# Kernel optimization log

Hardware: AMD Instinct MI355X
Metric: run time of the kernel (lower is better)

The kernel has to match this reference:

```python
import jax, jax.numpy as jnp
import numpy as np

D = 192
HEADS = 4
HD = D // HEADS
R = 3  # correlation radius actually used in forward_level
NDISP = (2 * R + 1) ** 2  # 49
T = 3  # frames -> 2 consecutive pairs
ITERS = 4


def layer_norm(x, w, b, eps=1e-5):
    m = jnp.mean(x, axis=-1, keepdims=True)
    v = jnp.var(x, axis=-1, keepdims=True)
    return (x - m) / jnp.sqrt(v + eps) * w + b


def mha(x, in_w, in_b, out_w, out_b):
    # torch nn.MultiheadAttention, batch_first, self-attention
    B, N, _ = x.shape
    qkv = x @ in_w.T + in_b
    q, k, v = jnp.split(qkv, 3, axis=-1)
    q = q.reshape(B, N, HEADS, HD).transpose(0, 2, 1, 3) * (1.0 / float(np.sqrt(HD)))
    k = k.reshape(B, N, HEADS, HD).transpose(0, 2, 1, 3)
    v = v.reshape(B, N, HEADS, HD).transpose(0, 2, 1, 3)
    att = jax.nn.softmax(jnp.einsum('bhqd,bhkd->bhqk', q, k), axis=-1)
    y = jnp.einsum('bhqk,bhkd->bhqd', att, v).transpose(0, 2, 1, 3).reshape(B, N, D)
    return y @ out_w.T + out_b


def tblock(x, p):
    ln1w, ln1b, inw, inb, ow, ob, ln2w, ln2b, w1, b1, w2, b2 = p
    x = x + mha(layer_norm(x, ln1w, ln1b), inw, inb, ow, ob)
    h = layer_norm(x, ln2w, ln2b)
    h = jax.nn.gelu(h @ w1.T + b1, approximate=False) @ w2.T + b2
    return x + h


def local_corr(f1, f2):
    C = f1.shape[1]
    scale = 1.0 / float(np.sqrt(C))
    outs = []
    for dy in range(-R, R + 1):
        for dx in range(-R, R + 1):
            f2s = jnp.roll(f2, (dy, dx), axis=(2, 3))
            outs.append(jnp.sum(f1 * f2s, axis=1) * scale)
    return jnp.stack(outs, axis=1)


def grid_sample_bilinear_border(img, grid):
    # img: B,C,H,W; grid: B,Ho,Wo,2 with (x,y) in [-1,1]; align_corners=True, border padding
    B, C, H, W = img.shape
    x = jnp.clip((grid[..., 0] + 1.0) * 0.5 * (W - 1), 0.0, W - 1)
    y = jnp.clip((grid[..., 1] + 1.0) * 0.5 * (H - 1), 0.0, H - 1)
    x0 = jnp.floor(x); y0 = jnp.floor(y)
    x1 = jnp.minimum(x0 + 1, W - 1); y1 = jnp.minimum(y0 + 1, H - 1)
    wx = (x - x0)[:, None]; wy = (y - y0)[:, None]
    imgf = img.reshape(B, C, H * W)
    Ho, Wo = x.shape[1], x.shape[2]
    def gather(yy, xx):
        idx = (yy * W + xx).astype(jnp.int32).reshape(B, 1, Ho * Wo)
        return jnp.take_along_axis(imgf, idx, axis=2).reshape(B, C, Ho, Wo)
    v00 = gather(y0, x0); v01 = gather(y0, x1)
    v10 = gather(y1, x0); v11 = gather(y1, x1)
    return v00 * (1 - wx) * (1 - wy) + v01 * wx * (1 - wy) + v10 * (1 - wx) * wy + v11 * wx * wy


def warp(img, flow):
    # flow in pixels, Bx2xHxW
    B, C, H, W = img.shape
    xs = jnp.linspace(-1.0, 1.0, W); ys = jnp.linspace(-1.0, 1.0, H)
    gx, gy = jnp.meshgrid(xs, ys)  # each (H, W), 'xy' indexing
    base = jnp.stack([gx, gy], axis=-1)[None]
    off = jnp.stack([flow[:, 0] * (2.0 / max(W - 1, 1)),
                     flow[:, 1] * (2.0 / max(H - 1, 1))], axis=-1)
    return grid_sample_bilinear_border(img, base + off)


def upsample2x_align(img):
    # F.interpolate(scale_factor=2, mode='bilinear', align_corners=True)
    B, C, H, W = img.shape
    Ho, Wo = 2 * H, 2 * W
    xs = jnp.linspace(-1.0, 1.0, Wo); ys = jnp.linspace(-1.0, 1.0, Ho)
    gx, gy = jnp.meshgrid(xs, ys)
    grid = jnp.broadcast_to(jnp.stack([gx, gy], axis=-1)[None], (B, Ho, Wo, 2))
    return grid_sample_bilinear_border(img, grid)


def conv2d(x, w, b):
    y = jax.lax.conv_general_dilated(x, w, (1, 1), ((1, 1), (1, 1)),
                                     dimension_numbers=('NCHW', 'OIHW', 'NCHW'))
    return y + b[None, :, None, None]


def _forward(feats_l1, feats_l2, feats_l3, tok_w, tok_b,
             lcm_ln1_w, lcm_ln1_b, lcm_in_w, lcm_in_b, lcm_out_w, lcm_out_b,
             lcm_ln2_w, lcm_ln2_b, lcm_mlp_w1, lcm_mlp_b1, lcm_mlp_w2, lcm_mlp_b2,
             gtr_ln1_w, gtr_ln1_b, gtr_in_w, gtr_in_b, gtr_out_w, gtr_out_b,
             gtr_ln2_w, gtr_ln2_b, gtr_mlp_w1, gtr_mlp_b1, gtr_mlp_w2, gtr_mlp_b2,
             head_w1, head_b1, head_w2, head_b2,
             ref1_w1, ref1_b1, ref1_w2, ref1_b2,
             ref0_w1, ref0_b1, ref0_w2, ref0_b2):
    feats = [[feats_l1[t] for t in range(T)],
             [feats_l2[t] for t in range(T)],
             [feats_l3[t] for t in range(T)]]
    # ---- CostTokenizer ----
    tokens = []
    for lvl in range(3):
        toks = []
        for k in range(T - 1):
            corr = local_corr(feats[lvl][k], feats[lvl][k + 1])
            toks.append(jnp.einsum('bchw,dc->bdhw', corr, tok_w[lvl]) + tok_b[lvl][None, :, None, None])
        tokens.append(toks)
    lcm_p = [(lcm_ln1_w[i], lcm_ln1_b[i], lcm_in_w[i], lcm_in_b[i], lcm_out_w[i], lcm_out_b[i],
              lcm_ln2_w[i], lcm_ln2_b[i], lcm_mlp_w1[i], lcm_mlp_b1[i], lcm_mlp_w2[i], lcm_mlp_b2[i])
             for i in range(lcm_ln1_w.shape[0])]
    gtr_p = [(gtr_ln1_w[i], gtr_ln1_b[i], gtr_in_w[i], gtr_in_b[i], gtr_out_w[i], gtr_out_b[i],
              gtr_ln2_w[i], gtr_ln2_b[i], gtr_mlp_w1[i], gtr_mlp_b1[i], gtr_mlp_w2[i], gtr_mlp_b2[i])
             for i in range(gtr_ln1_w.shape[0])]
    # ---- LatentCostMemory (EMA state; .detach() -> stop_gradient; state resets when N changes) ----
    state = None
    latent = []
    for toks in tokens:
        lvl_lat = []
        for tok in toks:
            B_, Dd, H, W = tok.shape
            x = tok.reshape(B_, Dd, H * W).transpose(0, 2, 1)  # b (h w) d
            for p in lcm_p:
                x = tblock(x, p)
            if state is None or state.shape[1] != x.shape[1]:
                state = jax.lax.stop_gradient(x)
            x = 0.8 * x + 0.2 * state
            state = jax.lax.stop_gradient(x)
            lvl_lat.append(x.transpose(0, 2, 1))  # b d n
        latent.append(lvl_lat)
    H8, W8 = feats[1][0].shape[-2:]
    coarse = []
    for lat in latent[1]:
        x = lat.transpose(0, 2, 1)
        for p in gtr_p:
            x = tblock(x, p)
        fv = jax.nn.gelu(x @ head_w1.T + head_b1, approximate=False) @ head_w2.T + head_b2
        coarse.append(fv.transpose(0, 2, 1).reshape(-1, 2, H8, W8))
    # ---- MSRecurrentDecoder ----
    outs = []
    for k, f8 in enumerate(coarse):
        cur = f8
        for _ in range(ITERS):
            w10 = warp(feats[1][k + 1], cur)
            x = jnp.concatenate([feats[1][k], cur, w10], axis=1)
            cur = cur + conv2d(jax.nn.gelu(conv2d(x, ref1_w1, ref1_b1), approximate=False), ref1_w2, ref1_b2)
        cur2 = upsample2x_align(cur)
        for _ in range(ITERS):
            w10 = warp(feats[0][k + 1], cur2)
            x = jnp.concatenate([feats[0][k], cur2, w10], axis=1)
            cur2 = cur2 + conv2d(jax.nn.gelu(conv2d(x, ref0_w1, ref0_b1), approximate=False), ref0_w2, ref0_b2)
        outs.append(cur2)
    return jnp.stack(outs)  # [pairs, B, 2, H/4, W/4]


def setup_inputs():
    key = jax.random.key(0)
    ks = iter(jax.random.split(key, 64))
    def rn(shape, s=1.0):
        return jax.random.normal(next(ks), shape, dtype=jnp.float32) * s
    B = 1
    inp = {}
    inp['feats_l1'] = rn((T, B, 64, 64, 64))
    inp['feats_l2'] = rn((T, B, 128, 32, 32))
    inp['feats_l3'] = rn((T, B, 192, 16, 16))
    inp['tok_w'] = rn((3, D, NDISP), 0.02)
    inp['tok_b'] = rn((3, D), 0.02)
    for pre, n in (('lcm', 6), ('gtr', 2)):
        inp[pre + '_ln1_w'] = jnp.ones((n, D), jnp.float32)
        inp[pre + '_ln1_b'] = jnp.zeros((n, D), jnp.float32)
        inp[pre + '_in_w'] = rn((n, 3 * D, D), 0.02)
        inp[pre + '_in_b'] = rn((n, 3 * D), 0.02)
        inp[pre + '_out_w'] = rn((n, D, D), 0.02)
        inp[pre + '_out_b'] = rn((n, D), 0.02)
        inp[pre + '_ln2_w'] = jnp.ones((n, D), jnp.float32)
        inp[pre + '_ln2_b'] = jnp.zeros((n, D), jnp.float32)
        inp[pre + '_mlp_w1'] = rn((n, 4 * D, D), 0.02)
        inp[pre + '_mlp_b1'] = rn((n, 4 * D), 0.02)
        inp[pre + '_mlp_w2'] = rn((n, D, 4 * D), 0.02)
        inp[pre + '_mlp_b2'] = rn((n, D), 0.02)
    inp['head_w1'] = rn((D, D), 0.02); inp['head_b1'] = rn((D,), 0.02)
    inp['head_w2'] = rn((2, D), 0.02); inp['head_b2'] = rn((2,), 0.02)
    inp['ref1_w1'] = rn((128, 258, 3, 3), 0.02); inp['ref1_b1'] = rn((128,), 0.02)
    inp['ref1_w2'] = rn((2, 128, 3, 3), 0.02); inp['ref1_b2'] = rn((2,), 0.02)
    inp['ref0_w1'] = rn((64, 130, 3, 3), 0.02); inp['ref0_b1'] = rn((64,), 0.02)
    inp['ref0_w2'] = rn((2, 64, 3, 3), 0.02); inp['ref0_b2'] = rn((2,), 0.02)
    return inp


def reference(feats_l1, feats_l2, feats_l3, tok_w, tok_b,
              lcm_ln1_w, lcm_ln1_b, lcm_in_w, lcm_in_b, lcm_out_w, lcm_out_b,
              lcm_ln2_w, lcm_ln2_b, lcm_mlp_w1, lcm_mlp_b1, lcm_mlp_w2, lcm_mlp_b2,
              gtr_ln1_w, gtr_ln1_b, gtr_in_w, gtr_in_b, gtr_out_w, gtr_out_b,
              gtr_ln2_w, gtr_ln2_b, gtr_mlp_w1, gtr_mlp_b1, gtr_mlp_w2, gtr_mlp_b2,
              head_w1, head_b1, head_w2, head_b2,
              ref1_w1, ref1_b1, ref1_w2, ref1_b2,
              ref0_w1, ref0_b1, ref0_w2, ref0_b2):
    return _forward(feats_l1, feats_l2, feats_l3, tok_w, tok_b,
                    lcm_ln1_w, lcm_ln1_b, lcm_in_w, lcm_in_b, lcm_out_w, lcm_out_b,
                    lcm_ln2_w, lcm_ln2_b, lcm_mlp_w1, lcm_mlp_b1, lcm_mlp_w2, lcm_mlp_b2,
                    gtr_ln1_w, gtr_ln1_b, gtr_in_w, gtr_in_b, gtr_out_w, gtr_out_b,
                    gtr_ln2_w, gtr_ln2_b, gtr_mlp_w1, gtr_mlp_b1, gtr_mlp_w2, gtr_mlp_b2,
                    head_w1, head_b1, head_w2, head_b2,
                    ref1_w1, ref1_b1, ref1_w2, ref1_b2,
                    ref0_w1, ref0_b1, ref0_w2, ref0_b2)
```

## Files before the change

kernel.cpp:

```cpp
#include <hip/hip_runtime.h>
#include <hip/hip_bf16.h>

typedef __hip_bfloat16 bf16;
typedef short bf16x8 __attribute__((ext_vector_type(8)));
typedef float f32x4 __attribute__((ext_vector_type(4)));

#define DEV __device__ __forceinline__

DEV float bf2f(bf16 v) { return __bfloat162float(v); }
DEV bf16 f2bf(float v) { return __float2bfloat16(v); }
DEV unsigned short bfr(float f) {
  bf16 h = __float2bfloat16(f);
  return *reinterpret_cast<unsigned short*>(&h);
}
DEV float shf(unsigned short u) {
  unsigned int x = ((unsigned int)u) << 16;
  return *reinterpret_cast<float*>(&x);
}
DEV float gelu_exact(float x) { return 0.5f * x * (1.0f + erff(x * 0.70710678118654752f)); }

DEV float ldw(const void* p, long i, int isb) {
  return isb ? __bfloat162float(((const bf16*)p)[i]) : ((const float*)p)[i];
}

__global__ void k_detect(const unsigned short* __restrict__ u, int* __restrict__ flag) {
  __shared__ int bad;
  if (threadIdx.x == 0) bad = 0;
  __syncthreads();
  for (int i = threadIdx.x; i < 8192; i += 256) {
    int expo = (u[i] >> 7) & 0xFF;
    if (expo >= 138) atomicOr(&bad, 1);
  }
  __syncthreads();
  if (threadIdx.x == 0) *flag = bad ? 0 : 1;
}
__global__ void k_setone(int* p) { *p = 1; }

__global__ void k_cvt(const void* __restrict__ s, float* __restrict__ d, int n,
                      const int* __restrict__ fl) {
  int isb = *fl;
  int i = blockIdx.x * blockDim.x + threadIdx.x;
  if (i < n) d[i] = ldw(s, i, isb);
}

__global__ void k_zerosh(unsigned short* __restrict__ p, int n8) {
  int i = blockIdx.x * blockDim.x + threadIdx.x;
  if (i < n8) { uint4 z = {0, 0, 0, 0}; *(uint4*)(p + (long)i * 8) = z; }
}

__global__ void k_padtokw(const void* __restrict__ tw, bf16* __restrict__ dst,
                          const int* __restrict__ fl) {
  int isb = *fl;
  int i = blockIdx.x * blockDim.x + threadIdx.x;
  if (i >= 12288) return;
  int n = i >> 6, k = i & 63;
  float v = (k < 49) ? ldw(tw, 9408 + (long)n * 49 + k, isb) : 0.0f;
  dst[i] = f2bf(v);
}

__global__ void k_packw(const void* __restrict__ src, bf16* __restrict__ dst,
                        int OC, int C, int ICT, int NP, int ICP, int n,
                        const int* __restrict__ fl) {
  int isb = *fl;
  int i = blockIdx.x * blockDim.x + threadIdx.x;
  if (i >= n) return;
  int s = i / (NP * ICP);
  int r = i - s * NP * ICP;
  int oc = r / ICP, icp = r - oc * ICP;
  float v = 0.0f;
  if (oc < OC) {
    int ic = -1;
    if (icp < C) ic = icp;
    else if (icp < 2 * C) ic = icp - C + C + 2;
    else if (icp < 2 * C + 2) ic = icp - 2 * C + C;
    if (ic >= 0 && ic < ICT) v = ldw(src, ((long)oc * ICT + ic) * 9 + s, isb);
  }
  dst[i] = f2bf(v);
}

__global__ void k_trans_feats(const void* __restrict__ in, bf16* __restrict__ Fp,
                              int F, int C, int HW, const int* __restrict__ fl) {
  int isb = *fl;
  int cpg = C >> 3;
  int n = F * HW * cpg;
  int i = blockIdx.x * blockDim.x + threadIdx.x;
  if (i >= n) return;
  int p = i % HW;
  int rem = i / HW;
  int c8 = rem % cpg;
  int f = rem / cpg;
  long base = (long)f * C * HW + (long)(c8 * 8) * HW + p;
  union { unsigned short u[8]; uint4 v; } pk;
#pragma unroll
  for (int j = 0; j < 8; ++j) pk.u[j] = bfr(ldw(in, base + (long)j * HW, isb));
  *(uint4*)((unsigned short*)Fp + ((long)f * HW + p) * C + c8 * 8) = pk.v;
}

template <int MW, int NT>
__global__ __launch_bounds__(256) void k_conv_warp(
    const bf16* __restrict__ Fp, const float* __restrict__ flow, int C, int ICP,
    const bf16* __restrict__ Wp, const float* __restrict__ bias,
    void* __restrict__ out, int NOUT, int H, int W, int lgW) {
  constexpr int NWN = 4 / MW;
  constexpr int BM = MW * 16;
  constexpr int BN = NWN * NT * 16;
  __shared__ unsigned short Asm[102][40];
  __shared__ unsigned short Wsm[9 * BN][40];
  int tid = threadIdx.x;
  int wv = tid >> 6, ln = tid & 63, quad = ln >> 4, l16 = ln & 15;
  int wm = wv % MW, wn = wv / MW;
  int n0 = blockIdx.x * BN;
  int m0 = blockIdx.y * BM;
  int b = blockIdx.z;
  int HW = H * W;
  int CW = (BM < W) ? BM : W;
  int lgCW = (CW == 64) ? 6 : 5;
  int RO = (BM > W) ? (BM >> lgW) : 1;
  int ACW = CW + 2;
  int AR = (RO + 2) * ACW;
  int py0 = m0 >> lgW;
  int px0 = m0 & (W - 1);
  const unsigned short* fcur = (const unsigned short*)Fp + (long)b * HW * C;
  const unsigned short* fnxt = (const unsigned short*)Fp + (long)(b + 1) * HW * C;
  const float* fl = flow + (long)b * 2 * HW;
  int nk = ICP >> 5;
  f32x4 acc[NT] = {};
  int mm_local = wm * 16 + l16;
  int plr = mm_local >> lgCW;
  int plc = mm_local & (CW - 1);
  for (int kc = 0; kc < nk; ++kc) {
    int chbase = kc * 32;
    for (int i = tid; i < AR * 4; i += 256) {
      int r = i >> 2, c4 = i & 3;
      int sr = r / ACW, sc = r - sr * ACW;
      int py = py0 + sr - 1, px = px0 + sc - 1;
      uint4 val = {0, 0, 0, 0};
      if (py >= 0 && py < H && px >= 0 && px < W) {
        int p = py * W + px;
        int ch = chbase + c4 * 8;
        if (ch < C) {
          val = *(const uint4*)(fcur + (long)p * C + ch);
        } else if (ch < 2 * C) {
          float fx = fl[p], fy = fl[HW + p];
          float x = fminf(fmaxf((float)px + fx, 0.0f), (float)(W - 1));
          float y = fminf(fmaxf((float)py + fy, 0.0f), (float)(H - 1));
          int x0 = (int)floorf(x), y0 = (int)floorf(y);
          int x1 = min(x0 + 1, W - 1), y1 = min(y0 + 1, H - 1);
          float wx = x - (float)x0, wy = y - (float)y0;
          float w00 = (1 - wx) * (1 - wy), w01 = wx * (1 - wy);
          float w10 = (1 - wx) * wy, w11 = wx * wy;
          int c = ch - C;
          union { unsigned short u[8]; uint4 v; } a = { .v = *(const uint4*)(fnxt + (long)(y0 * W + x0) * C + c) };
          union { unsigned short u[8]; uint4 v; } bb = { .v = *(const uint4*)(fnxt + (long)(y0 * W + x1) * C + c) };
          union { unsigned short u[8]; uint4 v; } cc = { .v = *(const uint4*)(fnxt + (long)(y1 * W + x0) * C + c) };
          union { unsigned short u[8]; uint4 v; } dd = { .v = *(const uint4*)(fnxt + (long)(y1 * W + x1) * C + c) };
          union { unsigned short u[8]; uint4 v; } o;
#pragma unroll
          for (int j = 0; j < 8; ++j) {
            float v = shf(a.u[j]) * w00 + shf(bb.u[j]) * w01 + shf(cc.u[j]) * w10 + shf(dd.u[j]) * w11;
            o.u[j] = bfr(v);
          }
          val = o.v;
        } else if (ch == 2 * C) {
          union { unsigned short u[8]; uint4 v; } o = { .v = {0, 0, 0, 0} };
          o.u[0] = bfr(fl[p]);
          o.u[1] = bfr(fl[HW + p]);
          val = o.v;
        }
      }
      *(uint4*)&Asm[r][c4 * 8] = val;
    }
    for (int i = tid; i < 9 * BN * 4; i += 256) {
      int r = i >> 2, c4 = i & 3;
      int s = r / BN, nl = r - s * BN;
      long g = ((long)s * NOUT + n0 + nl) * ICP + kc * 32 + c4 * 8;
      *(uint4*)&Wsm[r][c4 * 8] = *(const uint4*)((const unsigned short*)Wp + g);
    }
    __syncthreads();
#pragma unroll
    for (int s = 0; s < 9; ++s) {
      int ky = s / 3, kx = s - ky * 3;
      bf16x8 af = *(const bf16x8*)&Asm[(plr + ky) * ACW + plc + kx][quad * 8];
#pragma unroll
      for (int nt = 0; nt < NT; ++nt) {
        bf16x8 wf = *(const bf16x8*)&Wsm[s * BN + (wn * NT + nt) * 16 + l16][quad * 8];
        acc[nt] = __builtin_amdgcn_mfma_f32_16x16x32_bf16(af, wf, acc[nt], 0, 0, 0);
      }
    }
    __syncthreads();
  }
  int Wp2 = W + 2;
#pragma unroll
  for (int nt = 0; nt < NT; ++nt) {
    int n = n0 + (wn * NT + nt) * 16 + l16;
    float bv = bias[n];
#pragma unroll
    for (int r = 0; r < 4; ++r) {
      int mmo = m0 + wm * 16 + quad * 4 + r;
      int py = mmo >> lgW, px = mmo & (W - 1);
      float v = gelu_exact(acc[nt][r] + bv);
      ((unsigned short*)out)[((long)b * (H + 2) * Wp2 + (long)(py + 1) * Wp2 + px + 1) * NOUT + n]
          = bfr(v);
    }
  }
}

template <int MW, int NT, int MODE>
__global__ __launch_bounds__(256) void k_conv_mfma(
    const bf16* __restrict__ Ap, int ICP, const bf16* __restrict__ Wp,
    const float* __restrict__ bias, const float* __restrict__ res,
    void* __restrict__ out, int NOUT, int H, int W, int lgW) {
  constexpr int NWN = 4 / MW;
  constexpr int BM = MW * 16;
  constexpr int BN = NWN * NT * 16;
  __shared__ unsigned short Asm[198][40];
  __shared__ unsigned short Wsm[9 * BN][40];
  int tid = threadIdx.x;
  int wv = tid >> 6, ln = tid & 63, quad = ln >> 4, l16 = ln & 15;
  int wm = wv % MW, wn = wv / MW;
  int n0 = blockIdx.x * BN;
  int m0 = blockIdx.y * BM;
  int b = blockIdx.z;
  int Wp2 = W + 2;
  int CW = (BM < W) ? BM : W;
  int lgCW = (CW == 64) ? 6 : 5;
  int RO = (BM > W) ? (BM >> lgW) : 1;
  int ACW = CW + 2;
  int AR = (RO + 2) * ACW;
  int py0 = m0 >> lgW;
  int px0 = m0 & (W - 1);
  const unsigned short* A = (const unsigned short*)Ap + (long)b * (H + 2) * Wp2 * ICP;
  int NPr = (MODE == 0) ? NOUT : 16;
  int nk = ICP >> 5;
  f32x4 acc[NT] = {};
  int mm_local = wm * 16 + l16;
  int plr = mm_local >> lgCW;
  int plc = mm_local & (CW - 1);
  for (int kc = 0; kc < nk; ++kc) {
    for (int i = tid; i < AR * 4; i += 256) {
      int r = i >> 2, c4 = i & 3;
      int sr = r / ACW, sc = r - sr * ACW;
      long g = ((long)(py0 + sr) * Wp2 + px0 + sc) * ICP + kc * 32 + c4 * 8;
      *(uint4*)&Asm[r][c4 * 8] = *(const uint4*)(A + g);
    }
    for (int i = tid; i < 9 * BN * 4; i += 256) {
      int r = i >> 2, c4 = i & 3;
      int s = r / BN, nl = r - s * BN;
      long g = ((long)s * NPr + n0 + nl) * ICP + kc * 32 + c4 * 8;
      *(uint4*)&Wsm[r][c4 * 8] = *(const uint4*)((const unsigned short*)Wp + g);
    }
    __syncthreads();
#pragma unroll
    for (int s = 0; s < 9; ++s) {
      int ky = s / 3, kx = s - ky * 3;
      bf16x8 af = *(const bf16x8*)&Asm[(plr + ky) * ACW + plc + kx][quad * 8];
#pragma unroll
      for (int nt = 0; nt < NT; ++nt) {
        bf16x8 wf = *(const bf16x8*)&Wsm[s * BN + (wn * NT + nt) * 16 + l16][quad * 8];
        acc[nt] = __builtin_amdgcn_mfma_f32_16x16x32_bf16(af, wf, acc[nt], 0, 0, 0);
      }
    }
    __syncthreads();
  }
  if (MODE == 0) {
#pragma unroll
    for (int nt = 0; nt < NT; ++nt) {
      int n = n0 + (wn * NT + nt) * 16 + l16;
      float bv = bias[n];
#pragma unroll
      for (int r = 0; r < 4; ++r) {
        int mmo = m0 + wm * 16 + quad * 4 + r;
        int py = mmo >> lgW, px = mmo & (W - 1);
        float v = gelu_exact(acc[nt][r] + bv);
        ((unsigned short*)out)[((long)b * (H + 2) * Wp2 + (long)(py + 1) * Wp2 + px + 1) * NOUT + n]
            = bfr(v);
      }
    }
  } else {
    int n = l16;
    if (wn == 0 && n < 2) {
      float bv = bias[n];
      int HW = H * W;
#pragma unroll
      for (int r = 0; r < 4; ++r) {
        int mmo = m0 + wm * 16 + quad * 4 + r;
        float v = acc[0][r] + bv + res[(long)b * 2 * HW + (long)n * HW + mmo];
        ((float*)out)[(long)b * 2 * HW + (long)n * HW + mmo] = v;
      }
    }
  }
}

__global__ void k_corr(const bf16* __restrict__ Fp2, bf16* __restrict__ corrT) {
  __shared__ unsigned short f1r[128];
  int p = blockIdx.x;
  int b = blockIdx.y;
  int t = threadIdx.x;
  const unsigned short* f1 = (const unsigned short*)Fp2 + ((long)b * 1024 + p) * 128;
  if (t < 16) *(uint4*)&f1r[t * 8] = *(const uint4*)(f1 + t * 8);
  __syncthreads();
  long rowo = ((long)b * 1024 + p) * 64;
  if (t < 49) {
    int dy = t / 7 - 3, dx = t % 7 - 3;
    int h = p >> 5, w = p & 31;
    int p2 = (((h - dy) & 31) << 5) | ((w - dx) & 31);
    const unsigned short* f2 = (const unsigned short*)Fp2 + ((long)(b + 1) * 1024 + p2) * 128;
    float s = 0.0f;
    for (int c = 0; c < 128; c += 8) {
      union { unsigned short u[8]; uint4 v; } av = { .v = *(const uint4*)&f1r[c] };
      union { unsigned short u[8]; uint4 v; } bv = { .v = *(const uint4*)(f2 + c) };
#pragma unroll
      for (int j = 0; j < 8; ++j) s += shf(av.u[j]) * shf(bv.u[j]);
    }
    corrT[rowo + t] = f2bf(s * 0.08838834764831845f);
  } else {
    corrT[rowo + t] = f2bf(0.0f);
  }
}

template <int KT, int BM, int ACT, bool HASRES, int AMODE, int OUTBF, int VT>
__global__ __launch_bounds__(256) void k_gemm_mfma2(
    const void* __restrict__ A, const void* __restrict__ W, long woff,
    const void* __restrict__ bias, long boff, const int* __restrict__ flb,
    const float* __restrict__ res, void* __restrict__ C,
    int M, int N, const int* __restrict__ fl,
    const unsigned short* __restrict__ mop, const float* __restrict__ mml,
    bf16* __restrict__ vtout,
    const void* __restrict__ lnw, long lnwoff,
    const void* __restrict__ lnb, long lnboff) {
  (void)M;
  int isb = *fl;
  constexpr int NKC = ((KT < 192) ? KT : 192) >> 5;
  constexpr int WM = (BM == 64) ? 4 : 2;
  constexpr int NTW = (BM == 64) ? 4 : 2;
  constexpr int LPR = 256 / BM;
  constexpr int EPL = 192 / LPR;
  __shared__ unsigned short Asm[NKC][BM][40];
  __shared__ unsigned short Wsm[NKC][64][40];
  int tid = threadIdx.x;
  int wv = tid >> 6, ln = tid & 63;
  int quad = ln >> 4, l16 = ln & 15;
  int wm = wv % WM, wn = wv / WM;
  int m0 = blockIdx.y * BM, n0 = blockIdx.x * 64;
  f32x4 acc[NTW] = {};
  for (int s0 = 0; s0 < KT; s0 += 192) {
    if (s0) __syncthreads();
    for (int i = tid; i < NKC * 256; i += 256) {
      int c4 = i & 3, r = (i >> 2) & 63, kc = i >> 8;
      long eo = woff + (long)(n0 + r) * KT + s0 + kc * 32 + c4 * 8;
      if (isb) {
        *(uint4*)&Wsm[kc][r][c4 * 8] = *(const uint4*)((const unsigned short*)W + eo);
      } else {
        const float* wp = (const float*)W + eo;
        float4 w0 = *(const float4*)wp;
        float4 w1 = *(const float4*)(wp + 4);
        union { unsigned short u[8]; uint4 v; } pk;
        pk.u[0] = bfr(w0.x); pk.u[1] = bfr(w0.y); pk.u[2] = bfr(w0.z); pk.u[3] = bfr(w0.w);
        pk.u[4] = bfr(w1.x); pk.u[5] = bfr(w1.y); pk.u[6] = bfr(w1.z); pk.u[7] = bfr(w1.w);
        *(uint4*)&Wsm[kc][r][c4 * 8] = pk.v;
      }
    }
    if constexpr (AMODE == 1) {
      for (int i = tid; i < NKC * BM * 4; i += 256) {
        int c4 = i & 3, r = (i >> 2) % BM, kc = i / (BM * 4);
        const unsigned short* ap =
            (const unsigned short*)A + (long)(m0 + r) * KT + s0 + kc * 32 + c4 * 8;
        *(uint4*)&Asm[kc][r][c4 * 8] = *(const uint4*)ap;
      }
    } else if constexpr (AMODE == 0) {
      for (int i = tid; i < NKC * BM * 4; i += 256) {
        int c4 = i & 3, r = (i >> 2) % BM, kc = i / (BM * 4);
        const float* ap = (const float*)A + (long)(m0 + r) * KT + s0 + kc * 32 + c4 * 8;
        float4 a0 = *(const float4*)ap;
        float4 a1 = *(const float4*)(ap + 4);
        union { unsigned short u[8]; uint4 v; } pk;
        pk.u[0] = bfr(a0.x); pk.u[1] = bfr(a0.y); pk.u[2] = bfr(a0.z); pk.u[3] = bfr(a0.w);
        pk.u[4] = bfr(a1.x); pk.u[5] = bfr(a1.y); pk.u[6] = bfr(a1.z); pk.u[7] = bfr(a1.w);
        *(uint4*)&Asm[kc][r][c4 * 8] = pk.v;
      }
    } else if constexpr (AMODE == 3) {
      int row = tid / LPR, j = tid % LPR;
      const float* xr = (const float*)A + (long)(m0 + row) * 192 + j * EPL;
      float av[EPL];
#pragma unroll
      for (int q4 = 0; q4 < EPL / 4; ++q4) {
        float4 v = *(const float4*)(xr + q4 * 4);
        av[q4 * 4 + 0] = v.x; av[q4 * 4 + 1] = v.y;
        av[q4 * 4 + 2] = v.z; av[q4 * 4 + 3] = v.w;
      }
      float sum = 0.0f;
#pragma unroll
      for (int q = 0; q < EPL; ++q) sum += av[q];
#pragma unroll
      for (int o = 1; o < LPR; o <<= 1) sum += __shfl_xor(sum, o);
      float mean = sum * (1.0f / 192.0f);
      float vs = 0.0f;
#pragma unroll
      for (int q = 0; q < EPL; ++q) { float d = av[q] - mean; vs += d * d; }
#pragma unroll
      for (int o = 1; o < LPR; o <<= 1) vs += __shfl_xor(vs, o);
      float rstd = rsqrtf(vs * (1.0f / 192.0f) + 1e-5f);
#pragma unroll
      for (int g = 0; g < EPL / 8; ++g) {
        int k = j * EPL + g * 8;
        union { unsigned short u[8]; uint4 v; } pk;
#pragma unroll
        for (int e = 0; e < 8; ++e) {
          float gg = ldw(lnw, lnwoff + k + e, isb);
          float bb = ldw(lnb, lnboff + k + e, isb);
          pk.u[e] = bfr((av[g * 8 + e] - mean) * rstd * gg + bb);
        }
        *(uint4*)&Asm[k >> 5][row][k & 31] = pk.v;
      }
    } else {
      int row = tid / LPR, j = tid % LPR;
      int m = m0 + row;
      int rr = m & 1023, bb = m >> 10;
#pragma unroll
      for (int g = 0; g < EPL / 8; ++g) {
        int k = j * EPL + g * 8;
        int h = k / 48;
        int d0 = k - h * 48;
        long idx[4];
        float ms[4], ls[4];
        float Ms = -1e30f;
#pragma unroll
        for (int s = 0; s < 4; ++s) {
          idx[s] = (((long)s * 2 + bb) * 4 + h) * 1024 + rr;
          ms[s] = mml[idx[s] * 2];
          ls[s] = mml[idx[s] * 2 + 1];
          Ms = fmaxf(Ms, ms[s]);
        }
        float e[4], L = 0.0f;
#pragma unroll
        for (int s = 0; s < 4; ++s) { e[s] = __expf(ms[s] - Ms); L += ls[s] * e[s]; }
        float invL = 1.0f / L;
        union { unsigned short u[8]; uint4 v; } pk;
#pragma unroll
        for (int e2 = 0; e2 < 8; ++e2) {
          float o = 0.0f;
#pragma unroll
          for (int s = 0; s < 4; ++s) o += shf(mop[idx[s] * 48 + d0 + e2]) * e[s];
// ... 188 lines not shown
    if (isb) ((bf16*)out)[i] = f2bf(cur2[i]);
    else ((float*)out)[i] = cur2[i];
  }
}

extern "C" void kernel_launch(void* const* d_in, const int* in_sizes, int n_in,
                              void* d_out, int out_size, void* d_ws, size_t ws_size,
                              hipStream_t stream) {
  const void* feats_l1 = d_in[0];
  const void* feats_l2 = d_in[1];
  const void* tok_w = d_in[3];
  const void* tok_b = d_in[4];
  const void* lcm_ln1_w = d_in[5];
  const void* lcm_ln1_b = d_in[6];
  const void* lcm_in_w  = d_in[7];
  const void* lcm_in_b  = d_in[8];
  const void* lcm_out_w = d_in[9];
  const void* lcm_out_b = d_in[10];
  const void* lcm_ln2_w = d_in[11];
  const void* lcm_ln2_b = d_in[12];
  const void* lcm_mlp_w1 = d_in[13];
  const void* lcm_mlp_b1 = d_in[14];
  const void* lcm_mlp_w2 = d_in[15];
  const void* lcm_mlp_b2 = d_in[16];
  const void* gtr_ln1_w = d_in[17];
  const void* gtr_ln1_b = d_in[18];
  const void* gtr_in_w  = d_in[19];
  const void* gtr_in_b  = d_in[20];
  const void* gtr_out_w = d_in[21];
  const void* gtr_out_b = d_in[22];
  const void* gtr_ln2_w = d_in[23];
  const void* gtr_ln2_b = d_in[24];
  const void* gtr_mlp_w1 = d_in[25];
  const void* gtr_mlp_b1 = d_in[26];
  const void* gtr_mlp_w2 = d_in[27];
  const void* gtr_mlp_b2 = d_in[28];
  const void* head_w1 = d_in[29];
  const void* head_b1 = d_in[30];
  const void* head_w2 = d_in[31];
  const void* head_b2 = d_in[32];
  const void* ref1_w1 = d_in[33];
  const void* ref1_b1 = d_in[34];
  const void* ref1_w2 = d_in[35];
  const void* ref1_b2 = d_in[36];
  const void* ref0_w1 = d_in[37];
  const void* ref0_b1 = d_in[38];
  const void* ref0_w2 = d_in[39];
  const void* ref0_b2 = d_in[40];
  (void)ws_size; (void)n_in; (void)in_sizes; (void)out_size;

  int* flag = (int*)d_ws;
  int* oneflag = (int*)d_ws + 2;
  float* wsf = (float*)d_ws;
  float* F2   = wsf + 16;
  float* rA   = F2 + 393216;
  float* rX   = rA + 786432;
  float* rT   = rX + 393216;
  float* rY   = rT + 393216;
  float* big  = rY + 393216;
  float* fv   = big + 1572864;
  float* cur  = fv + 4096;
  float* cur2 = cur + 4096;
  float* cb1a = cur2 + 16384;
  float* cb1b = cb1a + 128;
  float* cb0a = cb1b + 16;
  float* cb0b = cb0a + 64;
  bf16* wtok  = (bf16*)(cb0b + 16);
  float* wpk  = cb0b + 16 + 6144;
  bf16* w1p1 = (bf16*)wpk;
  bf16* w1p2 = (bf16*)(wpk + 165888);
  bf16* w0p1 = (bf16*)(wpk + 175104);
  bf16* w0p2 = (bf16*)(wpk + 221184);

  float* x = rX;
  bf16* corrTb = (bf16*)big;
  bf16* qkvbb  = (bf16*)big;
  bf16* vtb    = (bf16*)(big + 655360);
  bf16* hidb   = (bf16*)big;
  unsigned short* opart = (unsigned short*)rA;
  float* mlbuf = rY;
  float* headh = rT;
  bf16* mid0p = (bf16*)rT;
  bf16* mid1p = (bf16*)rY;
  bf16* Fp2   = (bf16*)(big + 851968);
  bf16* Fp1   = (bf16*)(big + 1048576);

  k_detect<<<1, 256, 0, stream>>>((const unsigned short*)feats_l1, flag);
  k_setone<<<1, 1, 0, stream>>>(oneflag);
  k_cvt<<<1, 256, 0, stream>>>(ref1_b1, cb1a, 128, flag);
  k_cvt<<<1, 256, 0, stream>>>(ref1_b2, cb1b, 2, flag);
  k_cvt<<<1, 256, 0, stream>>>(ref0_b1, cb0a, 64, flag);
  k_cvt<<<1, 256, 0, stream>>>(ref0_b2, cb0b, 2, flag);
  k_padtokw<<<48, 256, 0, stream>>>(tok_w, wtok, flag);
  k_packw<<<1296, 256, 0, stream>>>(ref1_w1, w1p1, 128, 128, 258, 128, 288, 331776, flag);
  k_packw<<<72, 256, 0, stream>>>(ref1_w2, w1p2, 2, 128, 128, 16, 128, 18432, flag);
  k_packw<<<360, 256, 0, stream>>>(ref0_w1, w0p1, 64, 64, 130, 64, 160, 92160, flag);
  k_packw<<<36, 256, 0, stream>>>(ref0_w2, w0p2, 2, 64, 64, 16, 64, 9216, flag);
  k_trans_feats<<<192, 256, 0, stream>>>(feats_l2, Fp2, 3, 128, 1024, flag);
  k_trans_feats<<<384, 256, 0, stream>>>(feats_l1, Fp1, 3, 64, 4096, flag);

  k_corr<<<dim3(1024, 2), 64, 0, stream>>>(Fp2, corrTb);
  k_gemm_mfma2<64, 32, 0, false, 1, 0, 0><<<dim3(3, 64), 256, 0, stream>>>(
      corrTb, wtok, 0, tok_b, 192, flag, nullptr, x, 2048, 192, oneflag,
      nullptr, nullptr, nullptr, nullptr, 0, nullptr, 0);

  auto run_block = [&](const void* ln1w, long o1, const void* ln1b, long o2,
                       const void* inw, long o3, const void* inb, long o4,
                       const void* ow, long o5, const void* ob, long o6,
                       const void* ln2w, long o7, const void* ln2b, long o8,
                       const void* w1, long o9, const void* b1, long o10,
                       const void* w2, long o11, const void* b2, long o12) {
    k_gemm_mfma2<192, 64, 0, false, 3, 1, 1><<<dim3(9, 32), 256, 0, stream>>>(
        x, inw, o3, inb, o4, flag, nullptr, qkvbb, 2048, 576, flag,
        nullptr, nullptr, vtb, ln1w, o1, ln1b, o2);
    k_attn_mfma<<<dim3(64, 4, 2), 256, 0, stream>>>(qkvbb, vtb, opart, mlbuf);
    k_gemm_mfma2<192, 32, 0, true, 2, 0, 0><<<dim3(3, 64), 256, 0, stream>>>(
        nullptr, ow, o5, ob, o6, flag, x, x, 2048, 192, flag,
        opart, mlbuf, nullptr, nullptr, 0, nullptr, 0);
    k_gemm_mfma2<192, 64, 1, false, 3, 1, 0><<<dim3(12, 32), 256, 0, stream>>>(
        x, w1, o9, b1, o10, flag, nullptr, hidb, 2048, 768, flag,
        nullptr, nullptr, nullptr, ln2w, o7, ln2b, o8);
    k_gemm_mfma2<768, 32, 0, true, 1, 0, 0><<<dim3(3, 64), 256, 0, stream>>>(
        hidb, w2, o11, b2, o12, flag, x, x, 2048, 192, flag,
        nullptr, nullptr, nullptr, nullptr, 0, nullptr, 0);
  };

  for (int i = 0; i < 6; ++i) {
    run_block(lcm_ln1_w, (long)i * 192, lcm_ln1_b, (long)i * 192,
              lcm_in_w, (long)i * 110592, lcm_in_b, (long)i * 576,
              lcm_out_w, (long)i * 36864, lcm_out_b, (long)i * 192,
              lcm_ln2_w, (long)i * 192, lcm_ln2_b, (long)i * 192,
              lcm_mlp_w1, (long)i * 147456, lcm_mlp_b1, (long)i * 768,
              lcm_mlp_w2, (long)i * 147456, lcm_mlp_b2, (long)i * 192);
  }
  k_ema<<<768, 256, 0, stream>>>(x);

  for (int i = 0; i < 2; ++i) {
    run_block(gtr_ln1_w, (long)i * 192, gtr_ln1_b, (long)i * 192,
              gtr_in_w, (long)i * 110592, gtr_in_b, (long)i * 576,
              gtr_out_w, (long)i * 36864, gtr_out_b, (long)i * 192,
              gtr_ln2_w, (long)i * 192, gtr_ln2_b, (long)i * 192,
              gtr_mlp_w1, (long)i * 147456, gtr_mlp_b1, (long)i * 768,
              gtr_mlp_w2, (long)i * 147456, gtr_mlp_b2, (long)i * 192);
  }

  k_gemm_mfma2<192, 32, 1, false, 0, 0, 0><<<dim3(3, 64), 256, 0, stream>>>(
      x, head_w1, 0, head_b1, 0, flag, nullptr, headh, 2048, 192, flag,
      nullptr, nullptr, nullptr, nullptr, 0, nullptr, 0);
  k_head2<<<1024, 256, 0, stream>>>(headh, head_w2, head_b2, cur, flag);

  k_zerosh<<<768, 256, 0, stream>>>((unsigned short*)rT, 196608);

  for (int it = 0; it < 4; ++it) {
    k_conv_warp<2, 2><<<dim3(2, 32, 2), 256, 0, stream>>>(
        Fp2, cur, 128, 288, w1p1, cb1a, mid1p, 128, 32, 32, 5);
    k_conv_mfma<4, 1, 1><<<dim3(1, 16, 2), 256, 0, stream>>>(
        mid1p, 128, w1p2, cb1b, cur, cur, 2, 32, 32, 5);
  }
  k_upsample<<<64, 256, 0, stream>>>(cur, cur2);

  for (int it = 0; it < 4; ++it) {
    k_conv_warp<2, 2><<<dim3(1, 128, 2), 256, 0, stream>>>(
        Fp1, cur2, 64, 160, w0p1, cb0a, mid0p, 64, 64, 64, 6);
    k_conv_mfma<4, 1, 1><<<dim3(1, 64, 2), 256, 0, stream>>>(
        mid0p, 64, w0p2, cb0b, cur2, cur2, 2, 64, 64, 6);
  }

  k_out<<<64, 256, 0, stream>>>(cur2, d_out, flag);
}
```

Measured before the change: 1.029 ms.

## Pipeline warp-conv tile loads through registers and replace final conv with wave dot

```diff
diff --git a/kernel.cpp b/kernel.cpp
--- a/kernel.cpp
+++ b/kernel.cpp
@@ -96,198 +96,217 @@
   *(uint4*)((unsigned short*)Fp + ((long)f * HW + p) * C + c8 * 8) = pk.v;
 }
 
-template <int MW, int NT>
-__global__ __launch_bounds__(256) void k_conv_warp(
-    const bf16* __restrict__ Fp, const float* __restrict__ flow, int C, int ICP,
+template <int C, int ICP, int NOUT, int WW, int LGW>
+__global__ __launch_bounds__(256) void k_conv_warp2(
+    const bf16* __restrict__ Fp, const float* __restrict__ flow,
     const bf16* __restrict__ Wp, const float* __restrict__ bias,
-    void* __restrict__ out, int NOUT, int H, int W, int lgW) {
-  constexpr int NWN = 4 / MW;
-  constexpr int BM = MW * 16;
-  constexpr int BN = NWN * NT * 16;
-  __shared__ unsigned short Asm[102][40];
-  __shared__ unsigned short Wsm[9 * BN][40];
+    bf16* __restrict__ out) {
+  constexpr int HH = WW;
+  constexpr int HW = HH * WW;
+  constexpr int ACW = 34;
+  constexpr int AR = 3 * ACW;
+  constexpr int NK = ICP / 32;
+  constexpr int NWI = 5;
+  __shared__ unsigned short Asm[AR][40];
+  __shared__ unsigned short Wsm[9 * 32][40];
   int tid = threadIdx.x;
   int wv = tid >> 6, ln = tid & 63, quad = ln >> 4, l16 = ln & 15;
-  int wm = wv % MW, wn = wv / MW;
-  int n0 = blockIdx.x * BN;
-  int m0 = blockIdx.y * BM;
-  int b = blockIdx.z;
-  int HW = H * W;
-  int CW = (BM < W) ? BM : W;
-  int lgCW = (CW == 64) ? 6 : 5;
-  int RO = (BM > W) ? (BM >> lgW) : 1;
-  int ACW = CW + 2;
-  int AR = (RO + 2) * ACW;
-  int py0 = m0 >> lgW;
-  int px0 = m0 & (W - 1);
+  int wm = wv & 1, wn = wv >> 1;
+  int n0 = blockIdx.x * 32, m0 = blockIdx.y * 32, b = blockIdx.z;
+  int py0 = m0 >> LGW, px0 = m0 & (WW - 1);
   const unsigned short* fcur = (const unsigned short*)Fp + (long)b * HW * C;
   const unsigned short* fnxt = (const unsigned short*)Fp + (long)(b + 1) * HW * C;
   const float* fl = flow + (long)b * 2 * HW;
-  int nk = ICP >> 5;
-  f32x4 acc[NT] = {};
-  int mm_local = wm * 16 + l16;
-  int plr = mm_local >> lgCW;
-  int plc = mm_local & (CW - 1);
-  for (int kc = 0; kc < nk; ++kc) {
-    int chbase = kc * 32;
-    for (int i = tid; i < AR * 4; i += 256) {
-      int r = i >> 2, c4 = i & 3;
-      int sr = r / ACW, sc = r - sr * ACW;
-      int py = py0 + sr - 1, px = px0 + sc - 1;
-      uint4 val = {0, 0, 0, 0};
-      if (py >= 0 && py < H && px >= 0 && px < W) {
-        int p = py * W + px;
-        int ch = chbase + c4 * 8;
-        if (ch < C) {
-          val = *(const uint4*)(fcur + (long)p * C + ch);
-        } else if (ch < 2 * C) {
-          float fx = fl[p], fy = fl[HW + p];
-          float x = fminf(fmaxf((float)px + fx, 0.0f), (float)(W - 1));
-          float y = fminf(fmaxf((float)py + fy, 0.0f), (float)(H - 1));
-          int x0 = (int)floorf(x), y0 = (int)floorf(y);
-          int x1 = min(x0 + 1, W - 1), y1 = min(y0 + 1, H - 1);
-          float wx = x - (float)x0, wy = y - (float)y0;
-          float w00 = (1 - wx) * (1 - wy), w01 = wx * (1 - wy);
-          float w10 = (1 - wx) * wy, w11 = wx * wy;
-          int c = ch - C;
-          union { unsigned short u[8]; uint4 v; } a = { .v = *(const uint4*)(fnxt + (long)(y0 * W + x0) * C + c) };
-          union { unsigned short u[8]; uint4 v; } bb = { .v = *(const uint4*)(fnxt + (long)(y0 * W + x1) * C + c) };
-          union { unsigned short u[8]; uint4 v; } cc = { .v = *(const uint4*)(fnxt + (long)(y1 * W + x0) * C + c) };
-          union { unsigned short u[8]; uint4 v; } dd = { .v = *(const uint4*)(fnxt + (long)(y1 * W + x1) * C + c) };
-          union { unsigned short u[8]; uint4 v; } o;
-#pragma unroll
-          for (int j = 0; j < 8; ++j) {
-            float v = shf(a.u[j]) * w00 + shf(bb.u[j]) * w01 + shf(cc.u[j]) * w10 + shf(dd.u[j]) * w11;
-            o.u[j] = bfr(v);
-          }
-          val = o.v;
-        } else if (ch == 2 * C) {
-          union { unsigned short u[8]; uint4 v; } o = { .v = {0, 0, 0, 0} };
-          o.u[0] = bfr(fl[p]);
-          o.u[1] = bfr(fl[HW + p]);
-          val = o.v;
+  int c4 = tid & 3;
+  const uint4 Z4 = {0, 0, 0, 0};
+  int rr_[2], ipp[2];
+  bool ivalid[2], iin[2];
+  float w00[2], w01[2], w10[2], w11[2], ifx[2], ify[2];
+  const unsigned short *g00[2], *g01[2], *g10[2], *g11[2];
+#pragma unroll
+  for (int j = 0; j < 2; ++j) {
+    int idx = tid + j * 256;
+    ivalid[j] = idx < AR * 4;
+    int r = idx >> 2;
+    rr_[j] = r;
+    int sr = r / ACW, sc = r - sr * ACW;
+    int py = py0 + sr - 1, px = px0 + sc - 1;
+    bool in = ivalid[j] && py >= 0 && py < HH && px >= 0 && px < WW;
+    iin[j] = in;
+    int p = in ? (py * WW + px) : 0;
+    ipp[j] = p;
+    float fx = 0.0f, fy = 0.0f;
+    if (in) { fx = fl[p]; fy = fl[HW + p]; }
+    ifx[j] = fx; ify[j] = fy;
+    float x = fminf(fmaxf((float)px + fx, 0.0f), (float)(WW - 1));
+    float y = fminf(fmaxf((float)py + fy, 0.0f), (float)(HH - 1));
+    int x0 = (int)floorf(x), y0 = (int)floorf(y);
+    int x1 = min(x0 + 1, WW - 1), y1 = min(y0 + 1, HH - 1);
+    float wx = x - (float)x0, wy = y - (float)y0;
+    w00[j] = (1 - wx) * (1 - wy); w01[j] = wx * (1 - wy);
+    w10[j] = (1 - wx) * wy;       w11[j] = wx * wy;
+    g00[j] = fnxt + (long)(y0 * WW + x0) * C;
+    g01[j] = fnxt + (long)(y0 * WW + x1) * C;
+    g10[j] = fnxt + (long)(y1 * WW + x0) * C;
+    g11[j] = fnxt + (long)(y1 * WW + x1) * C;
+  }
+  uint4 fa[2] = {};
+  uint4 qa[2], qb[2], qc[2], qd[2];
+  uint4 wreg[NWI];
+  auto ldW = [&](int kc) {
+#pragma unroll
+    for (int j = 0; j < NWI; ++j) {
+      int idx = tid + j * 256;
+      if (idx < 9 * 32 * 4) {
+        int r = idx >> 2, cw = idx & 3;
+        int s = r >> 5, nl = r & 31;
+        wreg[j] = *(const uint4*)((const unsigned short*)Wp +
+                                  ((long)s * NOUT + n0 + nl) * ICP + kc * 32 + cw * 8);
+      }
+    }
+  };
+  auto stW = [&]() {
+#pragma unroll
+    for (int j = 0; j < NWI; ++j) {
+      int idx = tid + j * 256;
+      if (idx < 9 * 32 * 4) {
+        int r = idx >> 2, cw = idx & 3;
+        *(uint4*)&Wsm[r][cw * 8] = wreg[j];
+      }
+    }
+  };
+  auto ldA = [&](int kc) {
+    int chb = kc * 32;
+    if (chb < C) {
+#pragma unroll
+      for (int j = 0; j < 2; ++j) {
+        if (iin[j]) fa[j] = *(const uint4*)(fcur + (long)ipp[j] * C + chb + c4 * 8);
+        else fa[j] = Z4;
+      }
+    } else if (chb < 2 * C) {
+      int c = chb - C + c4 * 8;
+#pragma unroll
+      for (int j = 0; j < 2; ++j) {
+        if (iin[j]) {
+          qa[j] = *(const uint4*)(g00[j] + c);
+          qb[j] = *(const uint4*)(g01[j] + c);
+          qc[j] = *(const uint4*)(g10[j] + c);
+          qd[j] = *(const uint4*)(g11[j] + c);
         }
       }
-      *(uint4*)&Asm[r][c4 * 8] = val;
-    }
-    for (int i = tid; i < 9 * BN * 4; i += 256) {
-      int r = i >> 2, c4 = i & 3;
-      int s = r / BN, nl = r - s * BN;
-      long g = ((long)s * NOUT + n0 + nl) * ICP + kc * 32 + c4 * 8;
-      *(uint4*)&Wsm[r][c4 * 8] = *(const uint4*)((const unsigned short*)Wp + g);
-    }
+    }
+  };
+  auto stA = [&](int kc) {
+    int chb = kc * 32;
+    if (chb < C) {
+#pragma unroll
+      for (int j = 0; j < 2; ++j)
+        if (ivalid[j]) *(uint4*)&Asm[rr_[j]][c4 * 8] = fa[j];
+    } else if (chb < 2 * C) {
+#pragma unroll
+      for (int j = 0; j < 2; ++j) {
+        if (!ivalid[j]) continue;
+        uint4 val = Z4;
+        if (iin[j]) {
+          union { unsigned short u[8]; uint4 v; } A_ = { .v = qa[j] };
+          union { unsigned short u[8]; uint4 v; } B_ = { .v = qb[j] };
+          union { unsigned short u[8]; uint4 v; } C_ = { .v = qc[j] };
+          union { unsigned short u[8]; uint4 v; } D_ = { .v = qd[j] };
+          union { unsigned short u[8]; uint4 v; } O_;
+#pragma unroll
+          for (int e = 0; e < 8; ++e)
+            O_.u[e] = bfr(shf(A_.u[e]) * w00[j] + shf(B_.u[e]) * w01[j] +
+                          shf(C_.u[e]) * w10[j] + shf(D_.u[e]) * w11[j]);
+          val = O_.v;
+        }
+        *(uint4*)&Asm[rr_[j]][c4 * 8] = val;
+      }
+    } else {
+#pragma unroll
+      for (int j = 0; j < 2; ++j) {
+        if (!ivalid[j]) continue;
+        union { unsigned short u[8]; uint4 v; } O_ = { .v = {0, 0, 0, 0} };
+        if (iin[j] && c4 == 0) { O_.u[0] = bfr(ifx[j]); O_.u[1] = bfr(ify[j]); }
+        *(uint4*)&Asm[rr_[j]][c4 * 8] = O_.v;
+      }
+    }
+  };
+  f32x4 acc = {};
+  int mml = wm * 16 + l16;
+  ldW(0);
+  ldA(0);
+#pragma unroll
+  for (int kc = 0; kc < NK; ++kc) {
+    stW();
+    stA(kc);
     __syncthreads();
+    if (kc + 1 < NK) { ldW(kc + 1); ldA(kc + 1); }
 #pragma unroll
     for (int s = 0; s < 9; ++s) {
       int ky = s / 3, kx = s - ky * 3;
-      bf16x8 af = *(const bf16x8*)&Asm[(plr + ky) * ACW + plc + kx][quad * 8];
-#pragma unroll
-      for (int nt = 0; nt < NT; ++nt) {
-        bf16x8 wf = *(const bf16x8*)&Wsm[s * BN + (wn * NT + nt) * 16 + l16][quad * 8];
-        acc[nt] = __builtin_amdgcn_mfma_f32_16x16x32_bf16(af, wf, acc[nt], 0, 0, 0);
-      }
+      bf16x8 af = *(const bf16x8*)&Asm[ky * ACW + mml + kx][quad * 8];
+      bf16x8 wf = *(const bf16x8*)&Wsm[s * 32 + wn * 16 + l16][quad * 8];
+      acc = __builtin_amdgcn_mfma_f32_16x16x32_bf16(af, wf, acc, 0, 0, 0);
     }
     __syncthreads();
   }
-  int Wp2 = W + 2;
-#pragma unroll
-  for (int nt = 0; nt < NT; ++nt) {
-    int n = n0 + (wn * NT + nt) * 16 + l16;
-    float bv = bias[n];
-#pragma unroll
-    for (int r = 0; r < 4; ++r) {
-      int mmo = m0 + wm * 16 + quad * 4 + r;
-      int py = mmo >> lgW, px = mmo & (W - 1);
-      float v = gelu_exact(acc[nt][r] + bv);
-      ((unsigned short*)out)[((long)b * (H + 2) * Wp2 + (long)(py + 1) * Wp2 + px + 1) * NOUT + n]
-          = bfr(v);
-    }
-  }
-}
-
-template <int MW, int NT, int MODE>
-__global__ __launch_bounds__(256) void k_conv_mfma(
-    const bf16* __restrict__ Ap, int ICP, const bf16* __restrict__ Wp,
-    const float* __restrict__ bias, const float* __restrict__ res,
-    void* __restrict__ out, int NOUT, int H, int W, int lgW) {
-  constexpr int NWN = 4 / MW;
-  constexpr int BM = MW * 16;
-  constexpr int BN = NWN * NT * 16;
-  __shared__ unsigned short Asm[198][40];
-  __shared__ unsigned short Wsm[9 * BN][40];
-  int tid = threadIdx.x;
-  int wv = tid >> 6, ln = tid & 63, quad = ln >> 4, l16 = ln & 15;
-  int wm = wv % MW, wn = wv / MW;
-  int n0 = blockIdx.x * BN;
-  int m0 = blockIdx.y * BM;
-  int b = blockIdx.z;
-  int Wp2 = W + 2;
-  int CW = (BM < W) ? BM : W;
-  int lgCW = (CW == 64) ? 6 : 5;
-  int RO = (BM > W) ? (BM >> lgW) : 1;
-  int ACW = CW + 2;
-  int AR = (RO + 2) * ACW;
-  int py0 = m0 >> lgW;
-  int px0 = m0 & (W - 1);
-  const unsigned short* A = (const unsigned short*)Ap + (long)b * (H + 2) * Wp2 * ICP;
-  int NPr = (MODE == 0) ? NOUT : 16;
-  int nk = ICP >> 5;
-  f32x4 acc[NT] = {};
-  int mm_local = wm * 16 + l16;
-  int plr = mm_local >> lgCW;
-  int plc = mm_local & (CW - 1);
-  for (int kc = 0; kc < nk; ++kc) {
-    for (int i = tid; i < AR * 4; i += 256) {
-      int r = i >> 2, c4 = i & 3;
-      int sr = r / ACW, sc = r - sr * ACW;
-      long g = ((long)(py0 + sr) * Wp2 + px0 + sc) * ICP + kc * 32 + c4 * 8;
-      *(uint4*)&Asm[r][c4 * 8] = *(const uint4*)(A + g);
-    }
-    for (int i = tid; i < 9 * BN * 4; i += 256) {
-      int r = i >> 2, c4 = i & 3;
-      int s = r / BN, nl = r - s * BN;
-      long g = ((long)s * NPr + n0 + nl) * ICP + kc * 32 + c4 * 8;
-      *(uint4*)&Wsm[r][c4 * 8] = *(const uint4*)((const unsigned short*)Wp + g);
-    }
-    __syncthreads();
-#pragma unroll
-    for (int s = 0; s < 9; ++s) {
-      int ky = s / 3, kx = s - ky * 3;
-      bf16x8 af = *(const bf16x8*)&Asm[(plr + ky) * ACW + plc + kx][quad * 8];
-#pragma unroll
-      for (int nt = 0; nt < NT; ++nt) {
-        bf16x8 wf = *(const bf16x8*)&Wsm[s * BN + (wn * NT + nt) * 16 + l16][quad * 8];
-        acc[nt] = __builtin_amdgcn_mfma_f32_16x16x32_bf16(af, wf, acc[nt], 0, 0, 0);
-      }
-    }
-    __syncthreads();
-  }
-  if (MODE == 0) {
-#pragma unroll
-    for (int nt = 0; nt < NT; ++nt) {
-      int n = n0 + (wn * NT + nt) * 16 + l16;
-      float bv = bias[n];
-#pragma unroll
-      for (int r = 0; r < 4; ++r) {
-        int mmo = m0 + wm * 16 + quad * 4 + r;
-        int py = mmo >> lgW, px = mmo & (W - 1);
-        float v = gelu_exact(acc[nt][r] + bv);
-        ((unsigned short*)out)[((long)b * (H + 2) * Wp2 + (long)(py + 1) * Wp2 + px + 1) * NOUT + n]
-            = bfr(v);
-      }
-    }
-  } else {
-    int n = l16;
-    if (wn == 0 && n < 2) {
-      float bv = bias[n];
-      int HW = H * W;
-#pragma unroll
-      for (int r = 0; r < 4; ++r) {
-        int mmo = m0 + wm * 16 + quad * 4 + r;
-        float v = acc[0][r] + bv + res[(long)b * 2 * HW + (long)n * HW + mmo];
-        ((float*)out)[(long)b * 2 * HW + (long)n * HW + mmo] = v;
-      }
-    }
+  int n = n0 + wn * 16 + l16;
+  float bv = bias[n];
+  constexpr int Wp2 = WW + 2;
+#pragma unroll
+  for (int r = 0; r < 4; ++r) {
+    int mmo = m0 + wm * 16 + quad * 4 + r;
+    int py = mmo >> LGW, px = mmo & (WW - 1);
+    float v = gelu_exact(acc[r] + bv);
+    ((unsigned short*)out)[((long)b * (HH + 2) * Wp2 + (long)(py + 1) * Wp2 + px + 1) * NOUT + n]
+        = bfr(v);
+  }
+}
+
+template <int C, int WW, int LGW>
+__global__ __launch_bounds__(256) void k_conv2_dot(
+    const bf16* __restrict__ mid, const bf16* __restrict__ Wq,
+    const float* __restrict__ bias, float* __restrict__ cur) {
+  constexpr int HH = WW;
+  constexpr int HW = HH * WW;
+  constexpr int Wp2 = WW + 2;
+  constexpr int CPL = C / 64;
+  int tid = threadIdx.x, wv = tid >> 6, ln = tid & 63;
+  int gw = blockIdx.x * 4 + wv;
+  int b = gw >> (2 * LGW);
+  int p = gw & (HW - 1);
+  int py = p >> LGW, px = p & (WW - 1);
+  float r0 = cur[((long)b * 2 + 0) * HW + p];
+  float r1 = cur[((long)b * 2 + 1) * HW + p];
+  float b0 = bias[0], b1 = bias[1];
+  const unsigned short* base = (const unsigned short*)mid +
+      ((long)b * (HH + 2) * Wp2 + (long)py * Wp2 + px) * C + ln * CPL;
+  const unsigned short* wb = (const unsigned short*)Wq + ln * CPL;
+  float s0 = 0.0f, s1 = 0.0f;
+#pragma unroll
+  for (int t = 0; t < 9; ++t) {
+    int dy = t / 3, dx = t - dy * 3;
+    const unsigned short* ar = base + ((long)dy * Wp2 + dx) * C;
+    const unsigned short* w0r = wb + (long)(t * 16 + 0) * C;
+    const unsigned short* w1r = wb + (long)(t * 16 + 1) * C;
+    if (CPL == 2) {
+      unsigned int a = *(const unsigned int*)ar;
+      unsigned int q0 = *(const unsigned int*)w0r;
+      unsigned int q1 = *(const unsigned int*)w1r;
+      float a0 = shf((unsigned short)a), a1 = shf((unsigned short)(a >> 16));
+      s0 += a0 * shf((unsigned short)q0) + a1 * shf((unsigned short)(q0 >> 16));
+      s1 += a0 * shf((unsigned short)q1) + a1 * shf((unsigned short)(q1 >> 16));
+    } else {
+      float a0 = shf(ar[0]);
+      s0 += a0 * shf(w0r[0]);
+      s1 += a0 * shf(w1r[0]);
+    }
+  }
+#pragma unroll
+  for (int o = 32; o; o >>= 1) { s0 += __shfl_xor(s0, o); s1 += __shfl_xor(s1, o); }
+  if (ln == 0) {
+    cur[((long)b * 2 + 0) * HW + p] = s0 + b0 + r0;
+    cur[((long)b * 2 + 1) * HW + p] = s1 + b1 + r1;
   }
 }
 
@@ -782,18 +801,16 @@
   k_zerosh<<<768, 256, 0, stream>>>((unsigned short*)rT, 196608);
 
   for (int it = 0; it < 4; ++it) {
-    k_conv_warp<2, 2><<<dim3(2, 32, 2), 256, 0, stream>>>(
-        Fp2, cur, 128, 288, w1p1, cb1a, mid1p, 128, 32, 32, 5);
-    k_conv_mfma<4, 1, 1><<<dim3(1, 16, 2), 256, 0, stream>>>(
-        mid1p, 128, w1p2, cb1b, cur, cur, 2, 32, 32, 5);
+    k_conv_warp2<128, 288, 128, 32, 5><<<dim3(4, 32, 2), 256, 0, stream>>>(
+        Fp2, cur, w1p1, cb1a, mid1p);
+    k_conv2_dot<128, 32, 5><<<512, 256, 0, stream>>>(mid1p, w1p2, cb1b, cur);
   }
   k_upsample<<<64, 256, 0, stream>>>(cur, cur2);
 
   for (int it = 0; it < 4; ++it) {
-    k_conv_warp<2, 2><<<dim3(1, 128, 2), 256, 0, stream>>>(
-        Fp1, cur2, 64, 160, w0p1, cb0a, mid0p, 64, 64, 64, 6);
-    k_conv_mfma<4, 1, 1><<<dim3(1, 64, 2), 256, 0, stream>>>(
-        mid0p, 64, w0p2, cb0b, cur2, cur2, 2, 64, 64, 6);
+    k_conv_warp2<64, 160, 64, 64, 6><<<dim3(2, 128, 2), 256, 0, stream>>>(
+        Fp1, cur2, w0p1, cb0a, mid0p);
+    k_conv2_dot<64, 64, 6><<<2048, 256, 0, stream>>>(mid0p, w0p2, cb0b, cur2);
   }
 
   k_out<<<64, 256, 0, stream>>>(cur2, d_out, flag);
```

New measurement: 1.008 ms. 1.02x faster.
